# Kernel tuning notes

Hardware: AMD Instinct MI355X
Metric: run time of the kernel (lower is better)

Reference implementation:

```python
import jax, jax.numpy as jnp
import numpy as np

B, S, D = 2, 2048, 1024
H, KH = 16, 4            # query heads, kv heads
DK = D // H              # 64
REP = H // KH            # queries per kv head


def _rope(x):
    # x: (B, h, S, dk); non-interleaved rotate-half RoPE as in source
    dk = x.shape[-1]
    half = dk // 2
    seq = x.shape[2]
    theta = 10000.0 ** (-(jnp.arange(half, dtype=jnp.float32) / half))
    pos = jnp.arange(seq, dtype=jnp.float32)
    freqs = pos[:, None] * theta[None, :]          # (S, half)
    cos = jnp.cos(freqs)[None, None]               # (1,1,S,half)
    sin = jnp.sin(freqs)[None, None]
    x1, x2 = x[..., :half], x[..., half:]
    return jnp.concatenate([x1 * cos - x2 * sin, x2 * cos + x1 * sin], axis=-1)


def setup_inputs() -> dict:
    key = jax.random.key(0)
    ks = jax.random.split(key, 9)
    sd = 1.0 / np.sqrt(D)
    x = jax.random.normal(ks[0], (B, S, D), dtype=jnp.float32)
    # causal mask: 1 where attend allowed, 0 where masked (mask==0 -> -inf)
    mask = jnp.tril(jnp.ones((S, S), dtype=jnp.int32))[None, None]
    Wq = jax.random.normal(ks[1], (D, H * DK), dtype=jnp.float32) * sd
    bq = jnp.zeros((H * DK,), dtype=jnp.float32)
    Wk = jax.random.normal(ks[2], (D, KH * DK), dtype=jnp.float32) * sd
    bk = jnp.zeros((KH * DK,), dtype=jnp.float32)
    Wv = jax.random.normal(ks[3], (D, KH * DK), dtype=jnp.float32) * sd
    bv = jnp.zeros((KH * DK,), dtype=jnp.float32)
    Wo = jax.random.normal(ks[4], (H * DK, D), dtype=jnp.float32) * sd
    bo = jnp.zeros((D,), dtype=jnp.float32)
    return {"x": x, "mask": mask, "Wq": Wq, "bq": bq, "Wk": Wk, "bk": bk,
            "Wv": Wv, "bv": bv, "Wo": Wo, "bo": bo}


def reference(x, mask, Wq, bq, Wk, bk, Wv, bv, Wo, bo):
    b, s, _ = x.shape
    q = (x @ Wq + bq).reshape(b, s, H, DK).transpose(0, 2, 1, 3)   # (B,H,S,DK)
    k = (x @ Wk + bk).reshape(b, s, KH, DK).transpose(0, 2, 1, 3)  # (B,KH,S,DK)
    v = (x @ Wv + bv).reshape(b, s, KH, DK).transpose(0, 2, 1, 3)
    q = _rope(q)
    k = _rope(k)
    k = jnp.repeat(k, REP, axis=1)  # GQA expand: (B,H,S,DK)
    v = jnp.repeat(v, REP, axis=1)
    attn = jnp.einsum('bhqd,bhkd->bhqk', q, k) / np.sqrt(DK).astype(np.float32)
    attn = jnp.where(mask == 0, -jnp.inf, attn)
    score = jax.nn.softmax(attn, axis=-1)
    out = jnp.einsum('bhqk,bhkd->bhqd', score, v)   # (B,H,S,DK)
    out = out.transpose(0, 2, 1, 3).reshape(b, s, H * DK)
    return out @ Wo + bo
```

## Files before the change

kernel.cpp:

```cpp
#include <hip/hip_runtime.h>
#include <math.h>

#define B_   2
#define S_   2048
#define D_   1024
#define H_   16
#define KH_  4
#define DK_  64

using bf16x8 = __attribute__((ext_vector_type(8))) short;
using bf16x4 = __attribute__((ext_vector_type(4))) short;
using f32x4  = __attribute__((ext_vector_type(4))) float;
using f32x2  = __attribute__((ext_vector_type(2))) float;
using u32x4  = __attribute__((ext_vector_type(4))) unsigned int;
using u32x2  = __attribute__((ext_vector_type(2))) unsigned int;

__device__ inline unsigned short f2bf(float f) {
    unsigned u = __float_as_uint(f);
    u += 0x7FFFu + ((u >> 16) & 1u);
    return (unsigned short)(u >> 16);
}
__device__ inline float bf2f(unsigned short u) {
    return __uint_as_float(((unsigned)u) << 16);
}

#ifdef __has_builtin
#if __has_builtin(__builtin_amdgcn_cvt_pk_bf16_f32)
#define PKBF16 1
#endif
#if __has_builtin(__builtin_amdgcn_exp2f)
#define NEXP2 1
#endif
#endif
__device__ inline unsigned pk2bf(float a, float b) {
#ifdef PKBF16
    auto r = __builtin_amdgcn_cvt_pk_bf16_f32(a, b);
    unsigned u; __builtin_memcpy(&u, &r, 4);
    return u;
#else
    return (unsigned)f2bf(a) | ((unsigned)f2bf(b) << 16);
#endif
}
__device__ inline float fexp2(float x) {
#ifdef NEXP2
    return __builtin_amdgcn_exp2f(x);
#else
    return exp2f(x);
#endif
}

#define GL16(gp, lp) __builtin_amdgcn_global_load_lds( \
    (const __attribute__((address_space(1))) unsigned int*)(gp), \
    (__attribute__((address_space(3))) unsigned int*)(lp), 16, 0, 0)

__global__ __launch_bounds__(256) void prep_kernel(
    const float* __restrict__ x,
    const float* __restrict__ Wq, const float* __restrict__ Wk,
    const float* __restrict__ Wv, const float* __restrict__ Wo,
    unsigned short* __restrict__ xb,
    unsigned short* __restrict__ WqkvT,
    unsigned short* __restrict__ WoT,
    float* __restrict__ sct)
{
    __shared__ float T[64][65];
    const int t = threadIdx.x;
    int bx = blockIdx.x;

    if (bx < 2048) {
        const int i = bx * 256 + t;
        f32x4 a = *(const f32x4*)(x + (long)i * 8);
        f32x4 b = *(const f32x4*)(x + (long)i * 8 + 4);
        bf16x8 o;
        o[0] = (short)f2bf(a[0]); o[1] = (short)f2bf(a[1]);
        o[2] = (short)f2bf(a[2]); o[3] = (short)f2bf(a[3]);
        o[4] = (short)f2bf(b[0]); o[5] = (short)f2bf(b[1]);
        o[6] = (short)f2bf(b[2]); o[7] = (short)f2bf(b[3]);
        *(bf16x8*)(xb + (long)i * 8) = o;
        return;
    }
    if (bx >= 2688) {
        const int idx = (bx - 2688) * 256 + t;
        const int s = idx >> 5, d = idx & 31;
        const float theta = exp2f(-(float)d * (13.287712379549449f / 32.0f));
        const float f = (float)s * theta;
        sct[(long)idx * 2]     = cosf(f);
        sct[(long)idx * 2 + 1] = sinf(f);
        return;
    }
    bx -= 2048;
    const float* in; unsigned short* out; int C;
    if (bx < 256)      { in = Wq; out = WqkvT;               C = 1024; }
    else if (bx < 320) { in = Wk; out = WqkvT + 1024 * 1024; C = 256;  bx -= 256; }
    else if (bx < 384) { in = Wv; out = WqkvT + 1280 * 1024; C = 256;  bx -= 320; }
    else               { in = Wo; out = WoT;                 C = 1024; bx -= 384; }
    const int R  = 1024, nr = 16;
    const int r0 = (bx % nr) * 64;
    const int c0 = (bx / nr) * 64;
    {
        const int r  = t >> 2;
        const int cq = (t & 3) * 16;
        const float* src = in + (long)(r0 + r) * C + c0 + cq;
        #pragma unroll
        for (int i = 0; i < 4; ++i) {
            f32x4 v = *(const f32x4*)(src + i * 4);
            T[r][cq + i * 4 + 0] = v[0];
            T[r][cq + i * 4 + 1] = v[1];
            T[r][cq + i * 4 + 2] = v[2];
            T[r][cq + i * 4 + 3] = v[3];
        }
    }
    __syncthreads();
    {
        const int c  = t >> 2;
        const int rq = (t & 3) * 16;
        bf16x8 p0, p1;
        #pragma unroll
        for (int i = 0; i < 8; ++i) {
            p0[i] = (short)f2bf(T[rq + i][c]);
            p1[i] = (short)f2bf(T[rq + 8 + i][c]);
        }
        unsigned short* dst = out + (long)(c0 + c) * R + r0 + rq;
        *(bf16x8*)dst       = p0;
        *(bf16x8*)(dst + 8) = p1;
    }
}

template<bool BF16OUT>
__global__ __launch_bounds__(256) void gemm64_kernel(
    const unsigned short* __restrict__ A,
    const unsigned short* __restrict__ Bt,
    const float* __restrict__ b0,
    const float* __restrict__ b1,
    const float* __restrict__ b2,
    float* __restrict__ outf,
    unsigned short* __restrict__ outb,
    unsigned short* __restrict__ qbuf,
    unsigned short* __restrict__ kbuf,
    const float* __restrict__ sct,
    int N, int K)
{
    __shared__ unsigned short As[2][64][64];
    __shared__ unsigned short Bs[2][128][64];

    const int t  = threadIdx.x;
    const int m0 = blockIdx.x * 64;
    const int n0 = blockIdx.y * 128;

    const int w    = t >> 6;
    const int lane = t & 63;
    const int n    = lane & 15;
    const int quad = lane >> 4;
    const int wm   = (w >> 1) * 32;
    const int wn   = (w & 1) * 64;

    const int sr8 = lane >> 3;
    const int gch = (lane & 7) ^ sr8;

    const unsigned short* gA = A  + (long)(m0 + w * 8 + sr8) * K + gch * 8;
    const unsigned short* gB = Bt + (long)(n0 + w * 8 + sr8) * K + gch * 8;

    #define STAGE(buf, kk)                                              \
    do {                                                                \
        GL16(gA + (kk),              &As[buf][w * 8][0]);               \
        GL16(gA + 32 * K + (kk),     &As[buf][w * 8 + 32][0]);          \
        GL16(gB + (kk),              &Bs[buf][w * 8][0]);               \
        GL16(gB + 32 * K + (kk),     &Bs[buf][w * 8 + 32][0]);          \
        GL16(gB + 64 * K + (kk),     &Bs[buf][w * 8 + 64][0]);          \
        GL16(gB + 96 * K + (kk),     &Bs[buf][w * 8 + 96][0]);          \
    } while (0)

    STAGE(0, 0);

    f32x4 acc[2][4];
    #pragma unroll
    for (int i = 0; i < 2; ++i)
        #pragma unroll
        for (int j = 0; j < 4; ++j) acc[i][j] = 0.0f;

    const int n7 = n & 7;

    for (int k0 = 0; k0 < K; k0 += 64) {
        const int cur = (k0 >> 6) & 1;
        __syncthreads();
        if (k0 + 64 < K) STAGE(cur ^ 1, k0 + 64);

        #pragma unroll
        for (int kp = 0; kp < 2; ++kp) {
            const int ca = ((kp * 4 + quad) ^ n7) * 8;
            bf16x8 af[2], bfr[4];
            #pragma unroll
            for (int i = 0; i < 2; ++i)
                af[i] = *(const bf16x8*)&As[cur][wm + i * 16 + n][ca];
            #pragma unroll
            for (int j = 0; j < 4; ++j)
                bfr[j] = *(const bf16x8*)&Bs[cur][wn + j * 16 + n][ca];
            #pragma unroll
            for (int mi = 0; mi < 2; ++mi)
                #pragma unroll
                for (int ni = 0; ni < 4; ++ni)
                    acc[mi][ni] = __builtin_amdgcn_mfma_f32_16x16x32_bf16(
                        af[mi], bfr[ni], acc[mi][ni], 0, 0, 0);
        }
    }
    #undef STAGE

    if (BF16OUT) {
        const int colbase = n0 + wn;
        if (colbase < 1280) {
            const bool isQ = colbase < 1024;
            const float scl = isQ ? 0.1803368801111606f : 1.0f;
            const int hh = isQ ? (colbase >> 6) : ((colbase - 1024) >> 6);
            const int HH = isQ ? H_ : KH_;
            unsigned short* obase = isQ ? qbuf : kbuf;
            const int gn0 = colbase + n;
            const float bA = isQ ? b0[gn0]      : b1[gn0 - 1024];
            const float bB = isQ ? b0[gn0 + 16] : b1[gn0 - 1008];
            const float bC = isQ ? b0[gn0 + 32] : b1[gn0 - 992];
            const float bD = isQ ? b0[gn0 + 48] : b1[gn0 - 976];
            #pragma unroll
            for (int mi = 0; mi < 2; ++mi) {
                #pragma unroll
                for (int r = 0; r < 4; ++r) {
                    const int gm = m0 + wm + mi * 16 + quad * 4 + r;
                    const int bb = gm >> 11, s = gm & (S_ - 1);
                    const f32x2 t0 = *(const f32x2*)(sct + ((long)s * 32 + n) * 2);
                    const f32x2 t1 = *(const f32x2*)(sct + ((long)s * 32 + 16 + n) * 2);
                    const float c0 = t0[0] * scl, s0v = t0[1] * scl;
                    const float c1 = t1[0] * scl, s1v = t1[1] * scl;
                    const float x1 = acc[mi][0][r] + bA;
                    const float y1 = acc[mi][1][r] + bB;
                    const float x2 = acc[mi][2][r] + bC;
                    const float y2 = acc[mi][3][r] + bD;
                    unsigned short* dst =
                        obase + ((long)(bb * HH + hh) * S_ + s) * DK_;
                    dst[n]      = f2bf(x1 * c0 - x2 * s0v);
                    dst[16 + n] = f2bf(y1 * c1 - y2 * s1v);
                    dst[32 + n] = f2bf(x2 * c0 + x1 * s0v);
                    dst[48 + n] = f2bf(y2 * c1 + y1 * s1v);
                }
            }
        } else {
            #pragma unroll
            for (int mi = 0; mi < 2; ++mi) {
                #pragma unroll
                for (int r = 0; r < 4; ++r) {
                    const int gm = m0 + wm + mi * 16 + quad * 4 + r;
                    #pragma unroll
                    for (int ni = 0; ni < 4; ++ni) {
                        const int gn = colbase + ni * 16 + n;
                        outb[(long)gm * N + gn] =
                            f2bf(acc[mi][ni][r] + b2[gn - 1280]);
                    }
                }
            }
        }
    } else {
        #pragma unroll
        for (int mi = 0; mi < 2; ++mi) {
            #pragma unroll
            for (int r = 0; r < 4; ++r) {
                const int gm = m0 + wm + mi * 16 + quad * 4 + r;
                #pragma unroll
                for (int ni = 0; ni < 4; ++ni) {
                    const int gn = n0 + wn + ni * 16 + n;
                    outf[(long)gm * N + gn] = acc[mi][ni][r] + b0[gn];
                }
            }
        }
    }
}

__global__ __launch_bounds__(256) void scatter_kernel(
    const unsigned short* __restrict__ qkvm,
    unsigned short* __restrict__ vbuf)
{
    __shared__ unsigned short T[64][72];
    const int t = threadIdx.x;
    const int bx = blockIdx.x;
    const int bkh = bx >> 5;
    const int s0  = (bx & 31) * 64;
    {
        const int s  = t >> 2;
        const int dq = (t & 3) * 16;
        const unsigned short* src =
            qkvm + (long)((bkh >> 2) * S_ + s0 + s) * 1536 + 1280 + (bkh & 3) * 64 + dq;
        *(bf16x8*)&T[s][dq]     = *(const bf16x8*)src;
        *(bf16x8*)&T[s][dq + 8] = *(const bf16x8*)(src + 8);
    }
    __syncthreads();
    {
        const int d  = t >> 2;
        const int sq = (t & 3) * 16;
        bf16x8 p0, p1;
        #pragma unroll
        for (int i = 0; i < 8; ++i) {
            p0[i] = (short)T[sq + i][d];
            p1[i] = (short)T[sq + 8 + i][d];
        }
        unsigned short* dst = vbuf + ((long)bkh * DK_ + d) * S_ + s0 + sq;
        *(bf16x8*)dst       = p0;
        *(bf16x8*)(dst + 8) = p1;
    }
}

__global__ __launch_bounds__(512) void attn_kernel(
    const unsigned short* __restrict__ qb,
    const unsigned short* __restrict__ kbf,
    const unsigned short* __restrict__ vT,
    unsigned short* __restrict__ ot)
{
    __shared__ __align__(16) unsigned short Ks[2][64][64];
    __shared__ __align__(16) unsigned short Vs[2][64][64];
    __shared__ __align__(16) unsigned short Ps[8][16][64];

    const int tid = threadIdx.x;
    const int bx  = blockIdx.x;

    const int j  = bx >> 8;
    const int p  = bx & 255;
    const int g  = p >> 5;
    const int bh = p & 31;
    const int a  = j ? g : (15 - g);

    const int b   = bh >> 4, h = bh & 15;
    const int kh  = h >> 2;
    const int q0  = a * 128;

    const int wv   = tid >> 6;
    const int lane = tid & 63;
    const int n    = lane & 15;
    const int quad = lane >> 4;
    const int xk   = n & 7;

    const unsigned short* qp =
        qb + ((long)(b * H_ + h) * S_ + q0 + wv * 16 + n) * DK_;
    const bf16x8 qa0 = *(const bf16x8*)(qp + quad * 8);
    const bf16x8 qa1 = *(const bf16x8*)(qp + 32 + quad * 8);

    f32x4 O[4];
    #pragma unroll
    for (int dt = 0; dt < 4; ++dt) O[dt] = 0.0f;
    float lsum = 0.f;

    const unsigned short* kbase = kbf + (long)(b * KH_ + kh) * S_ * DK_;
    const unsigned short* vbase = vT  + (long)(b * KH_ + kh) * DK_ * S_;

    const int ntiles = 2 * a + 2;
    const int ub     = 2 * a + (wv >> 2);
    const int srow = tid >> 3;
    const int lc   = tid & 7;
    const int sc8  = lc * 8;
    const int pcs  = (lc ^ (srow & 7)) * 8;

    u32x4 kr = *(const u32x4*)(kbase + (long)srow * DK_ + sc8);
    u32x4 vr = *(const u32x4*)(vbase + (long)srow * S_ + sc8);
    *(u32x4*)&Ks[0][srow][pcs] = kr;
    *(u32x4*)&Vs[0][srow][pcs] = vr;

    for (int u = 0; u < ntiles; ++u) {
        const int cur = u & 1;
        const int kb  = u * 64;
        __syncthreads();

        if (u + 1 < ntiles) {
            const int kbn = kb + 64;
            kr = *(const u32x4*)(kbase + (long)(kbn + srow) * DK_ + sc8);
            vr = *(const u32x4*)(vbase + (long)srow * S_ + kbn + sc8);
        }

        if (u <= ub) {
            f32x4 sc[4];
            #pragma unroll
            for (int ct = 0; ct < 4; ++ct) {
                const bf16x8 kf0 =
                    *(const bf16x8*)&Ks[cur][ct * 16 + n][(quad ^ xk) * 8];
                const bf16x8 kf1 =
                    *(const bf16x8*)&Ks[cur][ct * 16 + n][((quad + 4) ^ xk) * 8];
                f32x4 c = 0.0f;
                c = __builtin_amdgcn_mfma_f32_16x16x32_bf16(kf0, qa0, c, 0, 0, 0);
                c = __builtin_amdgcn_mfma_f32_16x16x32_bf16(kf1, qa1, c, 0, 0, 0);
                sc[ct] = c;
            }

            if (u == ub) {
                const int qg = q0 + wv * 16 + n;
                #pragma unroll
                for (int ct = 0; ct < 4; ++ct) {
                    const int kq = kb + ct * 16 + quad * 4;
                    #pragma unroll
                    for (int r = 0; r < 4; ++r)
                        if (kq + r > qg) sc[ct][r] = -INFINITY;
                }
            }

            f32x4 rs4 = 0.0f;
            #pragma unroll
            for (int ct = 0; ct < 4; ++ct) {
                #pragma unroll
                for (int r = 0; r < 4; ++r) {
                    const float p2 = fexp2(sc[ct][r]);
                    sc[ct][r] = p2;
                    rs4[r] += p2;
                }
            }
            lsum += (rs4[0] + rs4[1]) + (rs4[2] + rs4[3]);

            #pragma unroll
            for (int ct = 0; ct < 4; ++ct) {
                u32x2 pw;
                pw[0] = pk2bf(sc[ct][0], sc[ct][1]);
                pw[1] = pk2bf(sc[ct][2], sc[ct][3]);
                const int pc = ((2 * ct + (quad >> 1)) ^ xk) * 8 + (quad & 1) * 4;
                *(u32x2*)&Ps[wv][n][pc] = pw;
            }
            const bf16x8 pb0 = *(const bf16x8*)&Ps[wv][n][(quad ^ xk) * 8];
            const bf16x8 pb1 = *(const bf16x8*)&Ps[wv][n][((quad + 4) ^ xk) * 8];

            #pragma unroll
            for (int dt = 0; dt < 4; ++dt) {
                const bf16x8 av0 =
                    *(const bf16x8*)&Vs[cur][dt * 16 + n][(quad ^ xk) * 8];
                const bf16x8 av1 =
                    *(const bf16x8*)&Vs[cur][dt * 16 + n][((quad + 4) ^ xk) * 8];
                O[dt] = __builtin_amdgcn_mfma_f32_16x16x32_bf16(av0, pb0, O[dt], 0, 0, 0);
                O[dt] = __builtin_amdgcn_mfma_f32_16x16x32_bf16(av1, pb1, O[dt], 0, 0, 0);
            }
        }

        if (u + 1 < ntiles) {
            const int nb = cur ^ 1;
            *(u32x4*)&Ks[nb][srow][pcs] = kr;
            *(u32x4*)&Vs[nb][srow][pcs] = vr;
        }
    }

    lsum += __shfl_xor(lsum, 16);
    lsum += __shfl_xor(lsum, 32);
    const float inv = 1.0f / lsum;
    #pragma unroll
    for (int dt = 0; dt < 4; ++dt) {
        u32x2 pw;
        pw[0] = pk2bf(O[dt][0] * inv, O[dt][1] * inv);
        pw[1] = pk2bf(O[dt][2] * inv, O[dt][3] * inv);
        const int pc = ((2 * dt + (quad >> 1)) ^ xk) * 8 + (quad & 1) * 4;
        *(u32x2*)&Ps[wv][n][pc] = pw;
    }
    __builtin_amdgcn_s_waitcnt(0);
    const int fr = lane >> 3;
    const int c8l = lane & 7;
    #pragma unroll
    for (int it = 0; it < 2; ++it) {
        const int row = it * 8 + fr;
        const int q   = q0 + wv * 16 + row;
        unsigned short* op = ot + ((long)(b * S_ + q) * H_ + h) * DK_ + c8l * 8;
        *(bf16x8*)op = *(const bf16x8*)&Ps[wv][row][(c8l ^ fr) * 8];
    }
}

extern "C" void kernel_launch(void* const* d_in, const int* in_sizes, int n_in,
                              void* d_out, int out_size, void* d_ws, size_t ws_size,
                              hipStream_t stream)
{
    const float* x  = (const float*)d_in[0];
    const float* Wq = (const float*)d_in[2];
    const float* bq = (const float*)d_in[3];
    const float* Wk = (const float*)d_in[4];
    const float* bk = (const float*)d_in[5];
    const float* Wv = (const float*)d_in[6];
    const float* bv = (const float*)d_in[7];
    const float* Wo = (const float*)d_in[8];
    const float* bo = (const float*)d_in[9];
    float* out = (float*)d_out;

    unsigned short* ws    = (unsigned short*)d_ws;
    unsigned short* xb    = ws;
    unsigned short* qkvm  = xb + 4194304;
    unsigned short* qbuf  = qkvm + 6291456;
    unsigned short* kbuf  = qbuf + 4194304;
    unsigned short* vbuf  = kbuf + 1048576;
    unsigned short* WqkvT = vbuf + 1048576;
    unsigned short* WoT   = WqkvT + 1572864;
    float*          sct   = (float*)(WoT + 1048576);
    unsigned short* ob    = qkvm;

    prep_kernel<<<2944, 256, 0, stream>>>(x, Wq, Wk, Wv, Wo, xb, WqkvT, WoT, sct);

    gemm64_kernel<true><<<dim3(64, 12), 256, 0, stream>>>(
        xb, WqkvT, bq, bk, bv, nullptr, qkvm, qbuf, kbuf, sct, 1536, 1024);

    scatter_kernel<<<256, 256, 0, stream>>>(qkvm, vbuf);

    attn_kernel<<<512, 512, 0, stream>>>(qbuf, kbuf, vbuf, ob);

    gemm64_kernel<false><<<dim3(64, 8), 256, 0, stream>>>(
        ob, WoT, bo, nullptr, nullptr, out, nullptr, nullptr, nullptr, nullptr,
        1024, 1024);
}
```

Measured before the change: 168.1 us.

## Keep P in registers by permuting V's key order in shared memory

Drops the round-trip of the softmax probabilities through the per-wave Ps shared buffer. P is packed directly from the score accumulators into MFMA B-operands, and V is stored in LDS with a matching permutation of the key dimension so the products still line up. This removes LDS stores and loads plus their latency from the inner loop. In exchange, the V tile is written as two 8-byte stores instead of one 16-byte store, and correctness depends on the permutation matching the MFMA output layout exactly.

```diff
diff --git a/kernel.cpp b/kernel.cpp
--- a/kernel.cpp
+++ b/kernel.cpp
@@ -350,12 +350,25 @@
     const int srow = tid >> 3;
     const int lc   = tid & 7;
     const int sc8  = lc * 8;
-    const int pcs  = (lc ^ (srow & 7)) * 8;
+    const int rk   = srow & 7;
+    const int pcs  = (lc ^ rk) * 8;
+
+    const int vb0  = (lc & 1) * 16 + ((lc >> 1) & 1) * 4 + (lc >> 2) * 32;
+    const int vc1  = vb0 >> 3;
+    const int voff = vb0 & 7;
+    const int vp1  = ((vc1 ^ rk) * 8) + voff;
+    const int vp2  = (((vc1 + 1) ^ rk) * 8) + voff;
 
     u32x4 kr = *(const u32x4*)(kbase + (long)srow * DK_ + sc8);
     u32x4 vr = *(const u32x4*)(vbase + (long)srow * S_ + sc8);
     *(u32x4*)&Ks[0][srow][pcs] = kr;
-    *(u32x4*)&Vs[0][srow][pcs] = vr;
+    {
+        u32x2 va, vb2;
+        va[0] = vr[0];  va[1] = vr[1];
+        vb2[0] = vr[2]; vb2[1] = vr[3];
+        *(u32x2*)&Vs[0][srow][vp1] = va;
+        *(u32x2*)&Vs[0][srow][vp2] = vb2;
+    }
 
     for (int u = 0; u < ntiles; ++u) {
         const int cur = u & 1;
@@ -405,16 +418,18 @@
             }
             lsum += (rs4[0] + rs4[1]) + (rs4[2] + rs4[3]);
 
-            #pragma unroll
-            for (int ct = 0; ct < 4; ++ct) {
-                u32x2 pw;
-                pw[0] = pk2bf(sc[ct][0], sc[ct][1]);
-                pw[1] = pk2bf(sc[ct][2], sc[ct][3]);
-                const int pc = ((2 * ct + (quad >> 1)) ^ xk) * 8 + (quad & 1) * 4;
-                *(u32x2*)&Ps[wv][n][pc] = pw;
-            }
-            const bf16x8 pb0 = *(const bf16x8*)&Ps[wv][n][(quad ^ xk) * 8];
-            const bf16x8 pb1 = *(const bf16x8*)&Ps[wv][n][((quad + 4) ^ xk) * 8];
+            u32x4 pw0, pw1;
+            pw0[0] = pk2bf(sc[0][0], sc[0][1]);
+            pw0[1] = pk2bf(sc[0][2], sc[0][3]);
+            pw0[2] = pk2bf(sc[1][0], sc[1][1]);
+            pw0[3] = pk2bf(sc[1][2], sc[1][3]);
+            pw1[0] = pk2bf(sc[2][0], sc[2][1]);
+            pw1[1] = pk2bf(sc[2][2], sc[2][3]);
+            pw1[2] = pk2bf(sc[3][0], sc[3][1]);
+            pw1[3] = pk2bf(sc[3][2], sc[3][3]);
+            bf16x8 pb0, pb1;
+            __builtin_memcpy(&pb0, &pw0, 16);
+            __builtin_memcpy(&pb1, &pw1, 16);
 
             #pragma unroll
             for (int dt = 0; dt < 4; ++dt) {
@@ -430,7 +445,11 @@
         if (u + 1 < ntiles) {
             const int nb = cur ^ 1;
             *(u32x4*)&Ks[nb][srow][pcs] = kr;
-            *(u32x4*)&Vs[nb][srow][pcs] = vr;
+            u32x2 va, vb2;
+            va[0] = vr[0];  va[1] = vr[1];
+            vb2[0] = vr[2]; vb2[1] = vr[3];
+            *(u32x2*)&Vs[nb][srow][vp1] = va;
+            *(u32x2*)&Vs[nb][srow][vp2] = vb2;
         }
     }
 
```

After: 168.3 us. Within noise of the previous version (+0.1%).
